# Performance work log

Hardware: AMD Instinct MI355X
Metric: run time of the kernel (lower is better)

Reference implementation:

```python
import jax, jax.numpy as jnp
import numpy as np

H = 16  # attention heads


def setup_inputs() -> dict:
    key = jax.random.key(0)
    k0, k1, k2 = jax.random.split(key, 3)
    B, T, C = 2, 2048, 1024
    x = jax.random.normal(k0, (B, T, C), dtype=jnp.float32)
    W_attn = jax.random.normal(k1, (3 * C, C), dtype=jnp.float32) * 0.02
    W_proj = jax.random.normal(k2, (C, C), dtype=jnp.float32) * 0.02
    b_proj = jnp.zeros((C,), dtype=jnp.float32)
    return {"x": x, "W_attn": W_attn, "W_proj": W_proj, "b_proj": b_proj}


def reference(x, W_attn, W_proj, b_proj):
    # Eval-mode (dropout = identity), rotational_embeddings=False, flash=False path.
    B, T, C = x.shape
    d = C // H
    qkv = jnp.einsum('btc,fc->btf', x, W_attn)          # [B,T,3C] fused QKV proj
    q, k, v = jnp.split(qkv, 3, axis=-1)
    # [B,T,C] -> [B,H,T,d]
    q = q.reshape(B, T, H, d).transpose(0, 2, 1, 3)
    k = k.reshape(B, T, H, d).transpose(0, 2, 1, 3)
    v = v.reshape(B, T, H, d).transpose(0, 2, 1, 3)
    scale = 1.0 / np.sqrt(d).astype(np.float32)
    att = jnp.einsum('bhqd,bhkd->bhqk', q, k) * scale    # full TxT scores (no mask)
    att = jax.nn.softmax(att, axis=-1)
    y = jnp.einsum('bhqk,bhkd->bhqd', att, v)            # [B,H,T,d]
    y = y.transpose(0, 2, 1, 3).reshape(B, T, C)
    return jnp.einsum('btc,oc->bto', y, W_proj) + b_proj
```

## Files before the change

kernel.cpp:

```cpp
#include <hip/hip_runtime.h>
#include <hip/hip_bf16.h>
#include <stdint.h>

typedef __attribute__((ext_vector_type(8))) short bf16x8;
typedef __attribute__((ext_vector_type(4))) float f32x4;

#define MFMA16(A,B,C) __builtin_amdgcn_mfma_f32_16x16x32_bf16(A,B,C,0,0,0)


__device__ inline void gld_lds16(const __hip_bfloat16* g, __hip_bfloat16* l) {
  __builtin_amdgcn_global_load_lds(
      (const __attribute__((address_space(1))) void*)g,
      (__attribute__((address_space(3))) void*)l, 16, 0, 0);
}

__global__ __launch_bounds__(256)
void cvt_bf16(const float* __restrict__ s0, __hip_bfloat16* __restrict__ d0, int n0,
              const float* __restrict__ s1, __hip_bfloat16* __restrict__ d1, int n1,
              const float* __restrict__ s2, __hip_bfloat16* __restrict__ d2, int n2)
{
  const float* s; __hip_bfloat16* d; int n;
  if      (blockIdx.y == 0) { s = s0; d = d0; n = n0; }
  else if (blockIdx.y == 1) { s = s1; d = d1; n = n1; }
  else                      { s = s2; d = d2; n = n2; }
  int idx = (blockIdx.x * 256 + threadIdx.x) * 8;
  if (idx >= n) return;
  float4 u0 = *(const float4*)(s + idx);
  float4 u1 = *(const float4*)(s + idx + 4);
  __hip_bfloat16 t[8];
  t[0] = __float2bfloat16(u0.x); t[1] = __float2bfloat16(u0.y);
  t[2] = __float2bfloat16(u0.z); t[3] = __float2bfloat16(u0.w);
  t[4] = __float2bfloat16(u1.x); t[5] = __float2bfloat16(u1.y);
  t[6] = __float2bfloat16(u1.z); t[7] = __float2bfloat16(u1.w);
  *(int4*)(d + idx) = *(const int4*)t;
}

template<typename TC>
__global__ __launch_bounds__(256)
void gemm_bt(const __hip_bfloat16* __restrict__ A,
             const __hip_bfloat16* __restrict__ B,
             TC* __restrict__ C,
             const float* __restrict__ bias,
             __hip_bfloat16* __restrict__ vtg,
             int M, int N, int K)
{
  __shared__ __align__(16) __hip_bfloat16 As[128 * 32];
  __shared__ __align__(16) __hip_bfloat16 Bs[128 * 32];

  const int tid  = threadIdx.x;
  const int lane = tid & 63;
  const int w    = tid >> 6;
  const int lm   = lane & 15;
  const int g    = lane >> 4;

  const int bm = blockIdx.y * 128;
  const int bn = blockIdx.x * 128;
  const int rm = (w >> 1) * 64;
  const int cn = (w & 1) * 64;

  const int row0 = tid >> 2;
  const int kc   = (tid & 3) * 8;

  const f32x4 fzero = {0.0f, 0.0f, 0.0f, 0.0f};
  f32x4 acc[4][4];
  for (int i = 0; i < 4; i++)
    for (int j = 0; j < 4; j++)
      acc[i][j] = fzero;

  for (int k0 = 0; k0 < K; k0 += 32) {
    __syncthreads();
    gld_lds16(&A[(size_t)(bm + row0)      * K + k0 + kc], &As[tid * 8]);
    gld_lds16(&A[(size_t)(bm + row0 + 64) * K + k0 + kc], &As[(tid + 256) * 8]);
    gld_lds16(&B[(size_t)(bn + row0)      * K + k0 + kc], &Bs[tid * 8]);
    gld_lds16(&B[(size_t)(bn + row0 + 64) * K + k0 + kc], &Bs[(tid + 256) * 8]);
    __syncthreads();

    bf16x8 af[4], bfr[4];
#pragma unroll
    for (int i = 0; i < 4; i++)
      af[i] = *(const bf16x8*)&As[(rm + 16 * i + lm) * 32 + 8 * g];
#pragma unroll
    for (int j = 0; j < 4; j++)
      bfr[j] = *(const bf16x8*)&Bs[(cn + 16 * j + lm) * 32 + 8 * g];
#pragma unroll
    for (int i = 0; i < 4; i++)
#pragma unroll
      for (int j = 0; j < 4; j++)
        acc[i][j] = MFMA16(af[i], bfr[j], acc[i][j]);
  }

  if (vtg != nullptr && bn >= 2048) {
#pragma unroll
    for (int j = 0; j < 4; j++) {
      int colv = bn + cn + 16 * j + lm - 2048;
      int vh = colv >> 6, dd = colv & 63;
#pragma unroll
      for (int i = 0; i < 4; i++) {
        int m0 = bm + rm + 16 * i + 4 * g;
        int bb = m0 >> 11, t0 = m0 & 2047;
        __hip_bfloat16 t4[4];
#pragma unroll
        for (int r = 0; r < 4; r++) t4[r] = __float2bfloat16(acc[i][j][r]);
        *(int2*)&vtg[((size_t)(bb * 16 + vh) * 64 + dd) * 2048 + t0] =
            *(const int2*)t4;
      }
    }
    return;
  }

#pragma unroll
  for (int j = 0; j < 4; j++) {
    int coln = bn + cn + 16 * j + lm;
    float bv = bias ? bias[coln] : 0.0f;
#pragma unroll
    for (int i = 0; i < 4; i++) {
#pragma unroll
      for (int r = 0; r < 4; r++) {
        int rowm = bm + rm + 16 * i + 4 * g + r;
        float v = acc[i][j][r] + bv;
        if constexpr (sizeof(TC) == 2)
          C[(size_t)rowm * N + coln] = __float2bfloat16(v);
        else
          C[(size_t)rowm * N + coln] = v;
      }
    }
  }
}

__global__ __launch_bounds__(256)
void mha(const __hip_bfloat16* __restrict__ qkv,
         const __hip_bfloat16* __restrict__ vtg,
         __hip_bfloat16* __restrict__ y)
{
  const int T = 2048, F = 3072, Cc = 1024;
  const int bh = blockIdx.x;
  const int b  = bh >> 4, h = bh & 15;
  const int qb0 = blockIdx.y * 128;

  const int tid  = threadIdx.x;
  const int lane = tid & 63;
  const int w    = tid >> 6;
  const int lm   = lane & 15;
  const int g    = lane >> 4;

  __shared__ __align__(16) __hip_bfloat16 Ks[2][64 * 64];
  __shared__ __align__(16) __hip_bfloat16 Vs[2][64 * 64];
  __shared__ __align__(16) __hip_bfloat16 Pld[4][32 * 72];

  const size_t rowbase = (size_t)b * T * F;
  const int hoff = h * 64;
  const __hip_bfloat16* Kbase = qkv + rowbase + 1024 + hoff;
  const __hip_bfloat16* Vtb   = vtg + (size_t)(b * 16 + h) * 64 * 2048;

  const int qw = qb0 + 32 * w;
  bf16x8 aq[2][2];
#pragma unroll
  for (int mt = 0; mt < 2; mt++)
#pragma unroll
    for (int kcq = 0; kcq < 2; kcq++)
      aq[mt][kcq] = *(const bf16x8*)
          &qkv[rowbase + (size_t)(qw + 16 * mt + lm) * F + hoff + 32 * kcq + 8 * g];

  const f32x4 fzero = {0.0f, 0.0f, 0.0f, 0.0f};
  f32x4 yacc[2][4];
  float lsum[2][4];
#pragma unroll
  for (int mt = 0; mt < 2; mt++) {
#pragma unroll
    for (int c = 0; c < 4; c++) yacc[mt][c] = fzero;
#pragma unroll
    for (int r = 0; r < 4; r++) lsum[mt][r] = 0.0f;
  }

  const int r0 = tid >> 3;
  const int sw = (tid & 7) ^ (r0 & 7);
  const int sx = lm & 7;

  gld_lds16(Kbase + (size_t)(0 + r0)       * F + sw * 8, &Ks[0][tid * 8]);
  gld_lds16(Kbase + (size_t)(0 + r0 + 32)  * F + sw * 8, &Ks[0][(tid + 256) * 8]);
  gld_lds16(Vtb   + (size_t)r0        * 2048 + 0 + sw * 8, &Vs[0][tid * 8]);
  gld_lds16(Vtb   + (size_t)(r0 + 32) * 2048 + 0 + sw * 8, &Vs[0][(tid + 256) * 8]);

  for (int t = 0; t < 32; t++) {
    const int buf = t & 1;
    __syncthreads();
    if (t + 1 < 32) {
      const int kvn = (t + 1) * 64;
      gld_lds16(Kbase + (size_t)(kvn + r0)      * F + sw * 8, &Ks[buf ^ 1][tid * 8]);
      gld_lds16(Kbase + (size_t)(kvn + r0 + 32) * F + sw * 8, &Ks[buf ^ 1][(tid + 256) * 8]);
      gld_lds16(Vtb + (size_t)r0        * 2048 + kvn + sw * 8, &Vs[buf ^ 1][tid * 8]);
      gld_lds16(Vtb + (size_t)(r0 + 32) * 2048 + kvn + sw * 8, &Vs[buf ^ 1][(tid + 256) * 8]);
    }

    f32x4 s[2][4];
#pragma unroll
    for (int c2 = 0; c2 < 4; c2++) {
      bf16x8 bk0 = *(const bf16x8*)&Ks[buf][(16 * c2 + lm) * 64 + ((0 + g) ^ sx) * 8];
      bf16x8 bk1 = *(const bf16x8*)&Ks[buf][(16 * c2 + lm) * 64 + ((4 + g) ^ sx) * 8];
#pragma unroll
      for (int mt = 0; mt < 2; mt++) {
        s[mt][c2] = MFMA16(aq[mt][0], bk0, fzero);
        s[mt][c2] = MFMA16(aq[mt][1], bk1, s[mt][c2]);
      }
    }

#pragma unroll
    for (int mt = 0; mt < 2; mt++)
#pragma unroll
      for (int c = 0; c < 4; c++)
#pragma unroll
        for (int r = 0; r < 4; r++) {
          float p = __expf(s[mt][c][r] * 0.125f);
          lsum[mt][r] += p;
          Pld[w][(16 * mt + 4 * g + r) * 72 + 16 * c + lm] = __float2bfloat16(p);
        }

    bf16x8 ap[2][2];
#pragma unroll
    for (int mt = 0; mt < 2; mt++)
#pragma unroll
      for (int kcp = 0; kcp < 2; kcp++)
        ap[mt][kcp] = *(const bf16x8*)&Pld[w][(16 * mt + lm) * 72 + 32 * kcp + 8 * g];
#pragma unroll
    for (int c = 0; c < 4; c++) {
#pragma unroll
      for (int e = 0; e < 2; e++) {
        bf16x8 bv = *(const bf16x8*)&Vs[buf][(16 * c + lm) * 64 + ((4 * e + g) ^ sx) * 8];
#pragma unroll
        for (int mt = 0; mt < 2; mt++)
          yacc[mt][c] = MFMA16(ap[mt][e], bv, yacc[mt][c]);
      }
    }
  }

#pragma unroll
  for (int mt = 0; mt < 2; mt++) {
    float rinv[4];
#pragma unroll
    for (int r = 0; r < 4; r++) {
      float ls = lsum[mt][r];
      ls += __shfl_xor(ls, 1);
      ls += __shfl_xor(ls, 2);
      ls += __shfl_xor(ls, 4);
      ls += __shfl_xor(ls, 8);
      rinv[r] = 1.0f / ls;
    }
#pragma unroll
    for (int c = 0; c < 4; c++)
#pragma unroll
      for (int r = 0; r < 4; r++) {
        int qrow = qw + 16 * mt + 4 * g + r;
        y[(size_t)(b * T + qrow) * Cc + hoff + 16 * c + lm] =
            __float2bfloat16(yacc[mt][c][r] * rinv[r]);
      }
  }
}

extern "C" void kernel_launch(void* const* d_in, const int* in_sizes, int n_in,
                              void* d_out, int out_size, void* d_ws, size_t ws_size,
                              hipStream_t stream)
{
  const float* x  = (const float*)d_in[0];
  const float* Wa = (const float*)d_in[1];
  const float* Wp = (const float*)d_in[2];
  const float* bp = (const float*)d_in[3];
  float* out = (float*)d_out;

  const int BT = 4096, C = 1024, F3 = 3072;
  char* ws = (char*)d_ws;
  __hip_bfloat16* qkv  = (__hip_bfloat16*)ws;
  __hip_bfloat16* vtg  = (__hip_bfloat16*)(ws + 25165824);
  __hip_bfloat16* xbf  = (__hip_bfloat16*)(ws + 33554432);
  __hip_bfloat16* yb   = xbf;
  __hip_bfloat16* Wabf = (__hip_bfloat16*)(ws + 41943040);
  __hip_bfloat16* Wpbf = (__hip_bfloat16*)(ws + 48234496);

  cvt_bf16<<<dim3(2048, 3), 256, 0, stream>>>(
      x, xbf, BT * C, Wa, Wabf, F3 * C, Wp, Wpbf, C * C);
  gemm_bt<__hip_bfloat16>
      <<<dim3(F3 / 128, BT / 128), 256, 0, stream>>>(xbf, Wabf, qkv, nullptr, vtg,
                                                     BT, F3, C);
  mha<<<dim3(32, 16), 256, 0, stream>>>(qkv, vtg, yb);
  gemm_bt<float>
      <<<dim3(C / 128, BT / 128), 256, 0, stream>>>(yb, Wpbf, out, bp, nullptr,
                                                    BT, C, C);
}
```

Measured before the change: 223.2 us.

## Split attention over KV halves with combine kernel; shrink projection GEMM tile

The attention kernel gains a grid z-dimension that splits the 2048 keys into two halves. Each half writes unnormalized bf16 partial outputs and fp32 row sums, and a new combine kernel adds the halves and normalizes them. This doubles the number of attention workgroups, so more of the GPU's compute units have work. The output-projection GEMM is templated and launched with 64x128 tiles, which doubles its block count for the same reason. The cost is an extra kernel launch, extra global traffic for the partials, and bf16 rounding of the unnormalized partial outputs. The split path runs only when the workspace is large enough.

```diff
diff --git a/kernel.cpp b/kernel.cpp
--- a/kernel.cpp
+++ b/kernel.cpp
@@ -35,7 +35,7 @@
   *(int4*)(d + idx) = *(const int4*)t;
 }
 
-template<typename TC>
+template<int BM, int BN, typename TC>
 __global__ __launch_bounds__(256)
 void gemm_bt(const __hip_bfloat16* __restrict__ A,
              const __hip_bfloat16* __restrict__ B,
@@ -44,8 +44,12 @@
              __hip_bfloat16* __restrict__ vtg,
              int M, int N, int K)
 {
-  __shared__ __align__(16) __hip_bfloat16 As[128 * 32];
-  __shared__ __align__(16) __hip_bfloat16 Bs[128 * 32];
+  constexpr int MI = BM / 32;
+  constexpr int NJ = BN / 32;
+  constexpr int NP = (BM + BN) / 64;
+
+  __shared__ __align__(16) __hip_bfloat16 As[BM * 32];
+  __shared__ __align__(16) __hip_bfloat16 Bs[BN * 32];
 
   const int tid  = threadIdx.x;
   const int lane = tid & 63;
@@ -53,49 +57,52 @@
   const int lm   = lane & 15;
   const int g    = lane >> 4;
 
-  const int bm = blockIdx.y * 128;
-  const int bn = blockIdx.x * 128;
-  const int rm = (w >> 1) * 64;
-  const int cn = (w & 1) * 64;
-
-  const int row0 = tid >> 2;
-  const int kc   = (tid & 3) * 8;
+  const int bm = blockIdx.y * BM;
+  const int bn = blockIdx.x * BN;
+  const int rm = (w >> 1) * (BM / 2);
+  const int cn = (w & 1) * (BN / 2);
 
   const f32x4 fzero = {0.0f, 0.0f, 0.0f, 0.0f};
-  f32x4 acc[4][4];
-  for (int i = 0; i < 4; i++)
-    for (int j = 0; j < 4; j++)
+  f32x4 acc[MI][NJ];
+  for (int i = 0; i < MI; i++)
+    for (int j = 0; j < NJ; j++)
       acc[i][j] = fzero;
 
   for (int k0 = 0; k0 < K; k0 += 32) {
     __syncthreads();
-    gld_lds16(&A[(size_t)(bm + row0)      * K + k0 + kc], &As[tid * 8]);
-    gld_lds16(&A[(size_t)(bm + row0 + 64) * K + k0 + kc], &As[(tid + 256) * 8]);
-    gld_lds16(&B[(size_t)(bn + row0)      * K + k0 + kc], &Bs[tid * 8]);
-    gld_lds16(&B[(size_t)(bn + row0 + 64) * K + k0 + kc], &Bs[(tid + 256) * 8]);
+#pragma unroll
+    for (int p = 0; p < NP; p++) {
+      int c = tid + p * 256;
+      if (c < BM * 4)
+        gld_lds16(&A[(size_t)(bm + (c >> 2)) * K + k0 + (c & 3) * 8], &As[c * 8]);
+      else {
+        int cb = c - BM * 4;
+        gld_lds16(&B[(size_t)(bn + (cb >> 2)) * K + k0 + (cb & 3) * 8], &Bs[cb * 8]);
+      }
+    }
     __syncthreads();
 
-    bf16x8 af[4], bfr[4];
-#pragma unroll
-    for (int i = 0; i < 4; i++)
+    bf16x8 af[MI], bfr[NJ];
+#pragma unroll
+    for (int i = 0; i < MI; i++)
       af[i] = *(const bf16x8*)&As[(rm + 16 * i + lm) * 32 + 8 * g];
 #pragma unroll
-    for (int j = 0; j < 4; j++)
+    for (int j = 0; j < NJ; j++)
       bfr[j] = *(const bf16x8*)&Bs[(cn + 16 * j + lm) * 32 + 8 * g];
 #pragma unroll
-    for (int i = 0; i < 4; i++)
-#pragma unroll
-      for (int j = 0; j < 4; j++)
+    for (int i = 0; i < MI; i++)
+#pragma unroll
+      for (int j = 0; j < NJ; j++)
         acc[i][j] = MFMA16(af[i], bfr[j], acc[i][j]);
   }
 
   if (vtg != nullptr && bn >= 2048) {
 #pragma unroll
-    for (int j = 0; j < 4; j++) {
+    for (int j = 0; j < NJ; j++) {
       int colv = bn + cn + 16 * j + lm - 2048;
       int vh = colv >> 6, dd = colv & 63;
 #pragma unroll
-      for (int i = 0; i < 4; i++) {
+      for (int i = 0; i < MI; i++) {
         int m0 = bm + rm + 16 * i + 4 * g;
         int bb = m0 >> 11, t0 = m0 & 2047;
         __hip_bfloat16 t4[4];
@@ -109,11 +116,11 @@
   }
 
 #pragma unroll
-  for (int j = 0; j < 4; j++) {
+  for (int j = 0; j < NJ; j++) {
     int coln = bn + cn + 16 * j + lm;
     float bv = bias ? bias[coln] : 0.0f;
 #pragma unroll
-    for (int i = 0; i < 4; i++) {
+    for (int i = 0; i < MI; i++) {
 #pragma unroll
       for (int r = 0; r < 4; r++) {
         int rowm = bm + rm + 16 * i + 4 * g + r;
@@ -130,12 +137,17 @@
 __global__ __launch_bounds__(256)
 void mha(const __hip_bfloat16* __restrict__ qkv,
          const __hip_bfloat16* __restrict__ vtg,
-         __hip_bfloat16* __restrict__ y)
+         __hip_bfloat16* __restrict__ yout,
+         __hip_bfloat16* __restrict__ po,
+         float* __restrict__ pl,
+         int nsteps)
 {
   const int T = 2048, F = 3072, Cc = 1024;
   const int bh = blockIdx.x;
   const int b  = bh >> 4, h = bh & 15;
   const int qb0 = blockIdx.y * 128;
+  const int z   = blockIdx.z;
+  const int kvb = z * 64 * nsteps;
 
   const int tid  = threadIdx.x;
   const int lane = tid & 63;
@@ -176,16 +188,16 @@
   const int sw = (tid & 7) ^ (r0 & 7);
   const int sx = lm & 7;
 
-  gld_lds16(Kbase + (size_t)(0 + r0)       * F + sw * 8, &Ks[0][tid * 8]);
-  gld_lds16(Kbase + (size_t)(0 + r0 + 32)  * F + sw * 8, &Ks[0][(tid + 256) * 8]);
-  gld_lds16(Vtb   + (size_t)r0        * 2048 + 0 + sw * 8, &Vs[0][tid * 8]);
-  gld_lds16(Vtb   + (size_t)(r0 + 32) * 2048 + 0 + sw * 8, &Vs[0][(tid + 256) * 8]);
-
-  for (int t = 0; t < 32; t++) {
+  gld_lds16(Kbase + (size_t)(kvb + r0)      * F + sw * 8, &Ks[0][tid * 8]);
+  gld_lds16(Kbase + (size_t)(kvb + r0 + 32) * F + sw * 8, &Ks[0][(tid + 256) * 8]);
+  gld_lds16(Vtb + (size_t)r0        * 2048 + kvb + sw * 8, &Vs[0][tid * 8]);
+  gld_lds16(Vtb + (size_t)(r0 + 32) * 2048 + kvb + sw * 8, &Vs[0][(tid + 256) * 8]);
+
+  for (int t = 0; t < nsteps; t++) {
     const int buf = t & 1;
     __syncthreads();
-    if (t + 1 < 32) {
-      const int kvn = (t + 1) * 64;
+    if (t + 1 < nsteps) {
+      const int kvn = kvb + (t + 1) * 64;
       gld_lds16(Kbase + (size_t)(kvn + r0)      * F + sw * 8, &Ks[buf ^ 1][tid * 8]);
       gld_lds16(Kbase + (size_t)(kvn + r0 + 32) * F + sw * 8, &Ks[buf ^ 1][(tid + 256) * 8]);
       gld_lds16(Vtb + (size_t)r0        * 2048 + kvn + sw * 8, &Vs[buf ^ 1][tid * 8]);
@@ -235,7 +247,7 @@
 
 #pragma unroll
   for (int mt = 0; mt < 2; mt++) {
-    float rinv[4];
+    float lred[4];
 #pragma unroll
     for (int r = 0; r < 4; r++) {
       float ls = lsum[mt][r];
@@ -243,17 +255,56 @@
       ls += __shfl_xor(ls, 2);
       ls += __shfl_xor(ls, 4);
       ls += __shfl_xor(ls, 8);
-      rinv[r] = 1.0f / ls;
-    }
-#pragma unroll
-    for (int c = 0; c < 4; c++)
-#pragma unroll
-      for (int r = 0; r < 4; r++) {
-        int qrow = qw + 16 * mt + 4 * g + r;
-        y[(size_t)(b * T + qrow) * Cc + hoff + 16 * c + lm] =
-            __float2bfloat16(yacc[mt][c][r] * rinv[r]);
-      }
-  }
+      lred[r] = ls;
+    }
+    if (yout != nullptr) {
+#pragma unroll
+      for (int c = 0; c < 4; c++)
+#pragma unroll
+        for (int r = 0; r < 4; r++) {
+          int qrow = qw + 16 * mt + 4 * g + r;
+          yout[(size_t)(b * T + qrow) * Cc + hoff + 16 * c + lm] =
+              __float2bfloat16(yacc[mt][c][r] / lred[r]);
+        }
+    } else {
+      __hip_bfloat16* pz = po + (size_t)z * 4096 * 1024;
+      float* plz = pl + (size_t)z * 4096 * 16;
+#pragma unroll
+      for (int c = 0; c < 4; c++)
+#pragma unroll
+        for (int r = 0; r < 4; r++) {
+          int qrow = qw + 16 * mt + 4 * g + r;
+          pz[(size_t)(b * T + qrow) * Cc + hoff + 16 * c + lm] =
+              __float2bfloat16(yacc[mt][c][r]);
+        }
+      if (lm == 0)
+#pragma unroll
+        for (int r = 0; r < 4; r++) {
+          int qrow = qw + 16 * mt + 4 * g + r;
+          plz[(b * T + qrow) * 16 + h] = lred[r];
+        }
+    }
+  }
+}
+
+__global__ __launch_bounds__(256)
+void combine(const __hip_bfloat16* __restrict__ po,
+             const float* __restrict__ pl,
+             __hip_bfloat16* __restrict__ y)
+{
+  int idx = (blockIdx.x * 256 + threadIdx.x) * 8;
+  int row = idx >> 10, c = idx & 1023, h = c >> 6;
+  float la = pl[row * 16 + h];
+  float lb = pl[4096 * 16 + row * 16 + h];
+  float rinv = 1.0f / (la + lb);
+  const __hip_bfloat16* pa = po + idx;
+  const __hip_bfloat16* pb = po + 4096 * 1024 + idx;
+  __hip_bfloat16 t[8];
+#pragma unroll
+  for (int j = 0; j < 8; j++)
+    t[j] = __float2bfloat16(
+        (__bfloat162float(pa[j]) + __bfloat162float(pb[j])) * rinv);
+  *(int4*)(y + idx) = *(const int4*)t;
 }
 
 extern "C" void kernel_launch(void* const* d_in, const int* in_sizes, int n_in,
@@ -274,14 +325,22 @@
   __hip_bfloat16* yb   = xbf;
   __hip_bfloat16* Wabf = (__hip_bfloat16*)(ws + 41943040);
   __hip_bfloat16* Wpbf = (__hip_bfloat16*)(ws + 48234496);
+  __hip_bfloat16* Opar = (__hip_bfloat16*)(ws + 50331648);
+  float*          lpar = (float*)(ws + 67108864);
+  const size_t need_split = 67633152;
 
   cvt_bf16<<<dim3(2048, 3), 256, 0, stream>>>(
       x, xbf, BT * C, Wa, Wabf, F3 * C, Wp, Wpbf, C * C);
-  gemm_bt<__hip_bfloat16>
+  gemm_bt<128, 128, __hip_bfloat16>
       <<<dim3(F3 / 128, BT / 128), 256, 0, stream>>>(xbf, Wabf, qkv, nullptr, vtg,
                                                      BT, F3, C);
-  mha<<<dim3(32, 16), 256, 0, stream>>>(qkv, vtg, yb);
-  gemm_bt<float>
-      <<<dim3(C / 128, BT / 128), 256, 0, stream>>>(yb, Wpbf, out, bp, nullptr,
-                                                    BT, C, C);
-}
+  if (ws_size >= need_split) {
+    mha<<<dim3(32, 16, 2), 256, 0, stream>>>(qkv, vtg, nullptr, Opar, lpar, 16);
+    combine<<<dim3(BT * C / 2048), 256, 0, stream>>>(Opar, lpar, yb);
+  } else {
+    mha<<<dim3(32, 16, 1), 256, 0, stream>>>(qkv, vtg, yb, nullptr, nullptr, 32);
+  }
+  gemm_bt<64, 128, float>
+      <<<dim3(C / 128, BT / 64), 256, 0, stream>>>(yb, Wpbf, out, bp, nullptr,
+                                                   BT, C, C);
+}
```

Result: no change. 221.2 us (-0.9%).
